# Kernel optimization log

Hardware: AMD Instinct MI355X
Metric: run time of the kernel (lower is better)

## Reference

```python
import jax, jax.numpy as jnp
import numpy as np

B, S, DIM, H = 2, 2048, 2048, 16
HD = DIM // H  # 128
ROPE_THETA = 10000.0
NEG = -1e9


def setup_inputs() -> dict:
    key = jax.random.key(0)
    ks = jax.random.split(key, 6)
    x = jax.random.normal(ks[0], (B, S, DIM), dtype=jnp.float32)
    # rotary embedding tables: angle[s, j] = s / theta^(2j/HD), j in [0, HD/2)
    inv_freq = 1.0 / (ROPE_THETA ** (jnp.arange(0, HD, 2, dtype=jnp.float32) / HD))
    angles = jnp.arange(S, dtype=jnp.float32)[:, None] * inv_freq[None, :]  # (S, HD/2)
    freqs_cos = jnp.cos(angles)
    freqs_sin = jnp.sin(angles)
    # causal additive mask (1,1,S,S)
    causal = jnp.tril(jnp.ones((S, S), dtype=jnp.bool_))
    mask = jnp.where(causal, 0.0, NEG).astype(jnp.float32)[None, None]
    sc = 1.0 / np.sqrt(DIM)
    wq = jax.random.normal(ks[1], (DIM, DIM), dtype=jnp.float32) * sc
    wk = jax.random.normal(ks[2], (DIM, DIM), dtype=jnp.float32) * sc
    wv = jax.random.normal(ks[3], (DIM, DIM), dtype=jnp.float32) * sc
    wo = jax.random.normal(ks[4], (DIM, DIM), dtype=jnp.float32) * sc
    return {"x": x, "freqs_cos": freqs_cos, "freqs_sin": freqs_sin,
            "mask": mask, "wq": wq, "wk": wk, "wv": wv, "wo": wo}


def _apply_rope(t, cos, sin):
    # t: (B,S,H,HD); cos/sin: (S, HD/2) -> broadcast (1,S,1,HD/2)
    tr = t[..., ::2]
    ti = t[..., 1::2]
    c = cos[None, :, None, :]
    s = sin[None, :, None, :]
    out_r = tr * c - ti * s
    out_i = tr * s + ti * c
    # interleave back: stack on last axis then flatten -> [r0,i0,r1,i1,...]
    return jnp.stack([out_r, out_i], axis=-1).reshape(t.shape)


def reference(x, freqs_cos, freqs_sin, mask, wq, wk, wv, wo):
    b, s, _ = x.shape
    xq = (x @ wq).reshape(b, s, H, HD)
    xk = (x @ wk).reshape(b, s, H, HD)
    xv = (x @ wv).reshape(b, s, H, HD)
    xq = _apply_rope(xq, freqs_cos, freqs_sin)
    xk = _apply_rope(xk, freqs_cos, freqs_sin)
    # (B,H,S,HD)
    q = jnp.transpose(xq, (0, 2, 1, 3)) * (1.0 / np.sqrt(HD))
    k = jnp.transpose(xk, (0, 2, 1, 3))
    v = jnp.transpose(xv, (0, 2, 1, 3))
    attn = jnp.einsum('bhqd,bhkd->bhqk', q, k) + mask[:, :, :s, :s]
    attn = jax.nn.softmax(attn, axis=-1)
    out = jnp.einsum('bhqk,bhkd->bhqd', attn, v)  # (B,H,S,HD)
    out = jnp.transpose(out, (0, 2, 1, 3)).reshape(b, s, H * HD)
    return out @ wo
```

## Files before the change

kernel.cpp:

```cpp
#include <hip/hip_runtime.h>
#include <hip/hip_bf16.h>
#include <cstdint>
#include <cstddef>

#define BB   2
#define SS   2048
#define DD   2048
#define HH   16
#define HDD  128

typedef unsigned short u16;
typedef __attribute__((ext_vector_type(8))) short short8;
typedef __attribute__((ext_vector_type(4))) float f32x4;

__device__ __forceinline__ u16 f2bf(float f) {
  union { float f; uint32_t u; } v; v.f = f;
  uint32_t r = v.u + 0x7fffu + ((v.u >> 16) & 1u);
  return (u16)(r >> 16);
}
__device__ __forceinline__ float bf2f(u16 b) {
  union { uint32_t u; float f; } v; v.u = ((uint32_t)b) << 16;
  return v.f;
}

__device__ __forceinline__ void gload16(const u16* g, u16* l) {
  __builtin_amdgcn_global_load_lds(
      (__attribute__((address_space(1))) void*)g,
      (__attribute__((address_space(3))) void*)l, 16, 0, 0);
}

__global__ void k_cvt(const float* __restrict__ x, u16* __restrict__ o) {
  int i = blockIdx.x * blockDim.x + threadIdx.x;
  const float4 v = reinterpret_cast<const float4*>(x)[i];
  uint2 p;
  p.x = (uint32_t)f2bf(v.x) | ((uint32_t)f2bf(v.y) << 16);
  p.y = (uint32_t)f2bf(v.z) | ((uint32_t)f2bf(v.w) << 16);
  reinterpret_cast<uint2*>(o)[i] = p;
}

__global__ void k_wt(const float* __restrict__ w, u16* __restrict__ wt) {
  __shared__ float t[32][33];
  const int n0 = blockIdx.x * 32, k0 = blockIdx.y * 32;
  const int tx = threadIdx.x, ty = threadIdx.y;
#pragma unroll
  for (int i = 0; i < 32; i += 8)
    t[ty + i][tx] = w[(size_t)(k0 + ty + i) * DD + n0 + tx];
  __syncthreads();
#pragma unroll
  for (int i = 0; i < 32; i += 8)
    wt[(size_t)(n0 + ty + i) * DD + k0 + tx] = f2bf(t[tx][ty + i]);
}

__global__ void k_vt(const u16* __restrict__ V, u16* __restrict__ Vt) {
  __shared__ u16 t[32][33];
  const int s0 = blockIdx.x * 32, d0 = blockIdx.y * 32, bh = blockIdx.z;
  const u16* vb = V + (size_t)bh * SS * HDD;
  u16* vt = Vt + (size_t)bh * SS * HDD;
  const int tx = threadIdx.x, ty = threadIdx.y;
#pragma unroll
  for (int i = 0; i < 32; i += 8)
    t[ty + i][tx] = vb[(size_t)(s0 + ty + i) * HDD + d0 + tx];
  __syncthreads();
#pragma unroll
  for (int i = 0; i < 32; i += 8)
    vt[(size_t)(d0 + ty + i) * SS + s0 + tx] = t[tx][ty + i];
}

__global__ void k_rope(u16* __restrict__ Q, u16* __restrict__ Kb,
                       const float* __restrict__ fc, const float* __restrict__ fs) {
  const int idx = blockIdx.x * blockDim.x + threadIdx.x;
  const int p = idx & 63;
  const int s = (idx >> 6) & (SS - 1);
  const float cv = fc[s * 64 + p], sv = fs[s * 64 + p];
  const size_t off = ((size_t)(idx >> 6)) * HDD + p * 2;
  const float sc = 0.08838834764831845f;
  const float qr = bf2f(Q[off]), qi = bf2f(Q[off + 1]);
  Q[off]      = f2bf((qr * cv - qi * sv) * sc);
  Q[off + 1]  = f2bf((qr * sv + qi * cv) * sc);
  const float kr = bf2f(Kb[off]), ki = bf2f(Kb[off + 1]);
  Kb[off]     = f2bf(kr * cv - ki * sv);
  Kb[off + 1] = f2bf(kr * sv + ki * cv);
}

template <int MODE>
__global__ __launch_bounds__(256) void k_gemm(const u16* __restrict__ A,
                                              const u16* __restrict__ Bt,
                                              void* __restrict__ out) {
  __shared__ __align__(16) u16 As[128 * 32];
  __shared__ __align__(16) u16 Bs[128 * 32];
  const int tid = threadIdx.x;
  const int wave = tid >> 6, lane = tid & 63;
  const int c = lane & 15, g = lane >> 4;
  const int row0 = blockIdx.x * 128, col0 = blockIdx.y * 128;
  const int wm = wave >> 1, wn = wave & 1;
  const int sr = lane >> 2;
  const int sk = (lane & 3) * 8;
  f32x4 acc[4][4] = {};
  for (int k0 = 0; k0 < DD; k0 += 32) {
#pragma unroll
    for (int r = 0; r < 2; ++r) {
      const int chunk = r * 4 + wave;
      const int row = chunk * 16 + sr;
      gload16(A  + (size_t)(row0 + row) * DD + k0 + sk, As + chunk * 512);
      gload16(Bt + (size_t)(col0 + row) * DD + k0 + sk, Bs + chunk * 512);
    }
    __syncthreads();
    short8 a[4], b[4];
#pragma unroll
    for (int i = 0; i < 4; ++i)
      a[i] = *reinterpret_cast<const short8*>(As + (wm * 64 + i * 16 + c) * 32 + g * 8);
#pragma unroll
    for (int j = 0; j < 4; ++j)
      b[j] = *reinterpret_cast<const short8*>(Bs + (wn * 64 + j * 16 + c) * 32 + g * 8);
#pragma unroll
    for (int i = 0; i < 4; ++i)
#pragma unroll
      for (int j = 0; j < 4; ++j)
        acc[i][j] = __builtin_amdgcn_mfma_f32_16x16x32_bf16(a[i], b[j], acc[i][j], 0, 0, 0);
    __syncthreads();
  }
#pragma unroll
  for (int i = 0; i < 4; ++i) {
#pragma unroll
    for (int j = 0; j < 4; ++j) {
      const int mb = row0 + wm * 64 + i * 16 + g * 4;
      const int n  = col0 + wn * 64 + j * 16 + c;
#pragma unroll
      for (int r = 0; r < 4; ++r) {
        const int m = mb + r;
        if (MODE == 0) {
          const int which = n >> 11;
          const int b_ = m >> 11, s_ = m & (SS - 1);
          const int h_ = (n >> 7) & 15, d_ = n & (HDD - 1);
          reinterpret_cast<u16*>(out)[(size_t)which * (BB * HH * SS * HDD) +
              (((size_t)(b_ * HH + h_)) * SS + s_) * HDD + d_] = f2bf(acc[i][j][r]);
        } else {
          reinterpret_cast<float*>(out)[(size_t)m * DD + n] = acc[i][j][r];
        }
      }
    }
  }
}

__global__ __launch_bounds__(256, 3) void k_attn(const u16* __restrict__ Q,
                                                 const u16* __restrict__ K,
                                                 const u16* __restrict__ Vt,
                                                 u16* __restrict__ O) {
  __shared__ __align__(16) u16 Kt[2][32 * 128];
  __shared__ __align__(16) u16 Vs[2][128 * 32];
  __shared__ __align__(16) u16 Pb[4 * 32 * 40];
  const int tid = threadIdx.x;
  const int wave = tid >> 6, lane = tid & 63;
  const int c = lane & 15, g = lane >> 4;
  const int l = blockIdx.x;
  int qi, bh;
  if (l < 256) { qi = 8 + (l & 7); bh = l >> 3; }
  else         { qi = 7 - ((l - 256) & 7); bh = (l - 256) >> 3; }
  const int q0 = qi * 128;
  const u16* Qp = Q  + (size_t)bh * SS * HDD;
  const u16* Kp = K  + (size_t)bh * SS * HDD;
  const u16* Vp = Vt + (size_t)bh * SS * HDD;
  short8 qf[2][4];
#pragma unroll
  for (int ms = 0; ms < 2; ++ms)
#pragma unroll
    for (int kd = 0; kd < 4; ++kd)
      qf[ms][kd] = *reinterpret_cast<const short8*>(
          Qp + (size_t)(q0 + wave * 32 + ms * 16 + c) * HDD + kd * 32 + g * 8);
  f32x4 acc[2][8] = {};
  float psum[2][4] = {};
  const int ntiles = (qi + 1) * 4;
  u16* pwav = Pb + wave * (32 * 40);
  const int krl = lane >> 4, kcl = lane & 15;
  const int vrl = lane >> 2, vcl = lane & 3;
  auto stage = [&](int t) {
    const int kv0 = t * 32;
    u16* kb = Kt[t & 1];
    u16* vb = Vs[t & 1];
#pragma unroll
    for (int j = 0; j < 2; ++j) {
      const int r0k = (j * 4 + wave) * 4;
      const int rowk = r0k + krl;
      gload16(Kp + (size_t)(kv0 + rowk) * HDD + ((kcl ^ (rowk & 15)) << 3),
              kb + r0k * 128);
      const int r0v = (j * 4 + wave) * 16;
      const int rowv = r0v + vrl;
      gload16(Vp + (size_t)rowv * SS + kv0 + ((vcl ^ (vrl & 3)) << 3),
              vb + r0v * 32);
    }
  };
  stage(0);
  for (int t = 0; t < ntiles; ++t) {
    __syncthreads();
    if (t + 1 < ntiles) stage(t + 1);
    const int kv0 = t * 32;
    const bool active = kv0 <= q0 + wave * 32 + 31;
    if (!active) continue;
    const u16* kb = Kt[t & 1];
    const u16* vv = Vs[t & 1];
    f32x4 s[2][2] = {};
#pragma unroll
    for (int ns = 0; ns < 2; ++ns)
#pragma unroll
      for (int kd = 0; kd < 4; ++kd) {
        const short8 b = *reinterpret_cast<const short8*>(
            kb + (ns * 16 + c) * 128 + (((kd * 4 + g) ^ c) << 3));
        s[0][ns] = __builtin_amdgcn_mfma_f32_16x16x32_bf16(qf[0][kd], b, s[0][ns], 0, 0, 0);
        s[1][ns] = __builtin_amdgcn_mfma_f32_16x16x32_bf16(qf[1][kd], b, s[1][ns], 0, 0, 0);
      }
#pragma unroll
    for (int ms = 0; ms < 2; ++ms) {
      const int qrow = q0 + wave * 32 + ms * 16 + g * 4;
#pragma unroll
      for (int r = 0; r < 4; ++r) {
        u16* pw = pwav + (ms * 16 + g * 4 + r) * 40 + c;
        float rs = 0.f;
#pragma unroll
        for (int ns = 0; ns < 2; ++ns) {
          const bool u = (kv0 + ns * 16 + c) <= (qrow + r);
          const float p = u ? __expf(s[ms][ns][r]) : 0.f;
          rs += p;
          pw[ns * 16] = f2bf(p);
        }
        psum[ms][r] += rs;
      }
    }
    short8 pa[2];
    pa[0] = *reinterpret_cast<const short8*>(pwav + c * 40 + g * 8);
    pa[1] = *reinterpret_cast<const short8*>(pwav + (16 + c) * 40 + g * 8);
#pragma unroll
    for (int nb = 0; nb < 8; ++nb) {
      const short8 vb2 = *reinterpret_cast<const short8*>(
          vv + (nb * 16 + c) * 32 + ((g ^ (c & 3)) << 3));
      acc[0][nb] = __builtin_amdgcn_mfma_f32_16x16x32_bf16(pa[0], vb2, acc[0][nb], 0, 0, 0);
      acc[1][nb] = __builtin_amdgcn_mfma_f32_16x16x32_bf16(pa[1], vb2, acc[1][nb], 0, 0, 0);
    }
  }
  const int b_ = bh >> 4, h_ = bh & 15;
#pragma unroll
  for (int ms = 0; ms < 2; ++ms) {
#pragma unroll
    for (int r = 0; r < 4; ++r) {
      float rs = psum[ms][r];
      rs += __shfl_xor(rs, 1);
      rs += __shfl_xor(rs, 2);
      rs += __shfl_xor(rs, 4);
      rs += __shfl_xor(rs, 8);
      const float inv = 1.f / rs;
      const int s_ = q0 + wave * 32 + ms * 16 + g * 4 + r;
      u16* op = O + ((size_t)(b_ * SS + s_)) * DD + h_ * HDD;
#pragma unroll
      for (int nb = 0; nb < 8; ++nb)
        op[nb * 16 + c] = f2bf(acc[ms][nb][r] * inv);
    }
  }
}

extern "C" void kernel_launch(void* const* d_in, const int* in_sizes, int n_in,
                              void* d_out, int out_size, void* d_ws, size_t ws_size,
                              hipStream_t stream) {
  const float* x  = (const float*)d_in[0];
  const float* fc = (const float*)d_in[1];
  const float* fs = (const float*)d_in[2];
  const float* wq = (const float*)d_in[4];
  const float* wk = (const float*)d_in[5];
  const float* wv = (const float*)d_in[6];
  const float* wo = (const float*)d_in[7];

  u16* ws  = (u16*)d_ws;
  u16* xb  = ws;
  u16* wqt = xb  + 8388608;
  u16* wkt = wqt + 4194304;
  u16* wvt = wkt + 4194304;
  u16* wot = wvt + 4194304;
  u16* Qb  = wot + 4194304;
  u16* Kb  = Qb  + 8388608;
  u16* Vb  = Kb  + 8388608;
  u16* Vtb = Vb  + 8388608;
  u16* ao  = Vtb + 8388608;

  const dim3 tb(32, 8);
  k_cvt<<<8192, 256, 0, stream>>>(x, xb);
  k_wt<<<dim3(64, 64), tb, 0, stream>>>(wq, wqt);
  k_wt<<<dim3(64, 64), tb, 0, stream>>>(wk, wkt);
  k_wt<<<dim3(64, 64), tb, 0, stream>>>(wv, wvt);
  k_wt<<<dim3(64, 64), tb, 0, stream>>>(wo, wot);
  k_gemm<0><<<dim3(32, 48), 256, 0, stream>>>(xb, wqt, (void*)Qb);
  k_rope<<<16384, 256, 0, stream>>>(Qb, Kb, fc, fs);
  k_vt<<<dim3(64, 4, 32), tb, 0, stream>>>(Vb, Vtb);
  k_attn<<<512, 256, 0, stream>>>(Qb, Kb, Vtb, ao);
  k_gemm<1><<<dim3(32, 16), 256, 0, stream>>>(ao, wot, d_out);
}
```

Baseline: 438.2 us.

## Fuse V transpose into QKV GEMM epilogue, merge weight transposes, swizzle GEMM LDS

The QKV GEMM epilogue now writes V directly in transposed (head, dim, seq) layout, which removes the separate V transpose kernel and its round trip through memory. The four weight transpose launches are merged into one launch with a z-dimension. The GEMM LDS layout gains an XOR swizzle on the k-chunk index to reduce bank conflicts on the short8 reads. The transposed V store is strided along seq per lane, so those epilogue writes are poorly coalesced.

```diff
diff --git a/kernel.cpp b/kernel.cpp
--- a/kernel.cpp
+++ b/kernel.cpp
@@ -8,6 +8,7 @@
 #define DD   2048
 #define HH   16
 #define HDD  128
+#define SEC  8388608
 
 typedef unsigned short u16;
 typedef __attribute__((ext_vector_type(8))) short short8;
@@ -38,8 +39,13 @@
   reinterpret_cast<uint2*>(o)[i] = p;
 }
 
-__global__ void k_wt(const float* __restrict__ w, u16* __restrict__ wt) {
+__global__ void k_wt4(const float* __restrict__ w0, const float* __restrict__ w1,
+                      const float* __restrict__ w2, const float* __restrict__ w3,
+                      u16* __restrict__ wt) {
   __shared__ float t[32][33];
+  const int z = blockIdx.z;
+  const float* w = (z == 0) ? w0 : (z == 1) ? w1 : (z == 2) ? w2 : w3;
+  u16* o = wt + (size_t)z * (DD * DD);
   const int n0 = blockIdx.x * 32, k0 = blockIdx.y * 32;
   const int tx = threadIdx.x, ty = threadIdx.y;
 #pragma unroll
@@ -48,22 +54,7 @@
   __syncthreads();
 #pragma unroll
   for (int i = 0; i < 32; i += 8)
-    wt[(size_t)(n0 + ty + i) * DD + k0 + tx] = f2bf(t[tx][ty + i]);
-}
-
-__global__ void k_vt(const u16* __restrict__ V, u16* __restrict__ Vt) {
-  __shared__ u16 t[32][33];
-  const int s0 = blockIdx.x * 32, d0 = blockIdx.y * 32, bh = blockIdx.z;
-  const u16* vb = V + (size_t)bh * SS * HDD;
-  u16* vt = Vt + (size_t)bh * SS * HDD;
-  const int tx = threadIdx.x, ty = threadIdx.y;
-#pragma unroll
-  for (int i = 0; i < 32; i += 8)
-    t[ty + i][tx] = vb[(size_t)(s0 + ty + i) * HDD + d0 + tx];
-  __syncthreads();
-#pragma unroll
-  for (int i = 0; i < 32; i += 8)
-    vt[(size_t)(d0 + ty + i) * SS + s0 + tx] = t[tx][ty + i];
+    o[(size_t)(n0 + ty + i) * DD + k0 + tx] = f2bf(t[tx][ty + i]);
 }
 
 __global__ void k_rope(u16* __restrict__ Q, u16* __restrict__ Kb,
@@ -94,7 +85,7 @@
   const int row0 = blockIdx.x * 128, col0 = blockIdx.y * 128;
   const int wm = wave >> 1, wn = wave & 1;
   const int sr = lane >> 2;
-  const int sk = (lane & 3) * 8;
+  const int sk = (((lane & 3) ^ ((lane >> 3) & 3))) * 8;
   f32x4 acc[4][4] = {};
   for (int k0 = 0; k0 < DD; k0 += 32) {
 #pragma unroll
@@ -106,12 +97,13 @@
     }
     __syncthreads();
     short8 a[4], b[4];
+    const int gq = (g ^ ((c >> 1) & 3)) * 8;
 #pragma unroll
     for (int i = 0; i < 4; ++i)
-      a[i] = *reinterpret_cast<const short8*>(As + (wm * 64 + i * 16 + c) * 32 + g * 8);
+      a[i] = *reinterpret_cast<const short8*>(As + (wm * 64 + i * 16 + c) * 32 + gq);
 #pragma unroll
     for (int j = 0; j < 4; ++j)
-      b[j] = *reinterpret_cast<const short8*>(Bs + (wn * 64 + j * 16 + c) * 32 + g * 8);
+      b[j] = *reinterpret_cast<const short8*>(Bs + (wn * 64 + j * 16 + c) * 32 + gq);
 #pragma unroll
     for (int i = 0; i < 4; ++i)
 #pragma unroll
@@ -132,8 +124,12 @@
           const int which = n >> 11;
           const int b_ = m >> 11, s_ = m & (SS - 1);
           const int h_ = (n >> 7) & 15, d_ = n & (HDD - 1);
-          reinterpret_cast<u16*>(out)[(size_t)which * (BB * HH * SS * HDD) +
-              (((size_t)(b_ * HH + h_)) * SS + s_) * HDD + d_] = f2bf(acc[i][j][r]);
+          size_t idx;
+          if (which == 2)
+            idx = 2 * (size_t)SEC + (((size_t)(b_ * HH + h_)) * HDD + d_) * SS + s_;
+          else
+            idx = (size_t)which * SEC + (((size_t)(b_ * HH + h_)) * SS + s_) * HDD + d_;
+          reinterpret_cast<u16*>(out)[idx] = f2bf(acc[i][j][r]);
         } else {
           reinterpret_cast<float*>(out)[(size_t)m * DD + n] = acc[i][j][r];
         }
@@ -270,24 +266,16 @@
   u16* ws  = (u16*)d_ws;
   u16* xb  = ws;
   u16* wqt = xb  + 8388608;
-  u16* wkt = wqt + 4194304;
-  u16* wvt = wkt + 4194304;
-  u16* wot = wvt + 4194304;
+  u16* wot = wqt + 3 * 4194304;
   u16* Qb  = wot + 4194304;
-  u16* Kb  = Qb  + 8388608;
-  u16* Vb  = Kb  + 8388608;
-  u16* Vtb = Vb  + 8388608;
-  u16* ao  = Vtb + 8388608;
-
-  const dim3 tb(32, 8);
+  u16* Kb  = Qb  + SEC;
+  u16* Vtb = Kb  + SEC;
+  u16* ao  = Vtb + SEC;
+
   k_cvt<<<8192, 256, 0, stream>>>(x, xb);
-  k_wt<<<dim3(64, 64), tb, 0, stream>>>(wq, wqt);
-  k_wt<<<dim3(64, 64), tb, 0, stream>>>(wk, wkt);
-  k_wt<<<dim3(64, 64), tb, 0, stream>>>(wv, wvt);
-  k_wt<<<dim3(64, 64), tb, 0, stream>>>(wo, wot);
+  k_wt4<<<dim3(64, 64, 4), dim3(32, 8), 0, stream>>>(wq, wk, wv, wo, wqt);
   k_gemm<0><<<dim3(32, 48), 256, 0, stream>>>(xb, wqt, (void*)Qb);
   k_rope<<<16384, 256, 0, stream>>>(Qb, Kb, fc, fs);
-  k_vt<<<dim3(64, 4, 32), tb, 0, stream>>>(Vb, Vtb);
   k_attn<<<512, 256, 0, stream>>>(Qb, Kb, Vtb, ao);
   k_gemm<1><<<dim3(32, 16), 256, 0, stream>>>(ao, wot, d_out);
 }
```

After: 450.9 us. 2.9% more time.
